# Optimization experiments

Measured on AMD Instinct MI355X. Metric: run time of the kernel, lower is better.

Reference implementation:

```python
import jax, jax.numpy as jnp
import numpy as np

NEG_SLOPE = 0.2

def gat_conv(x, src, dst, W, a_src, a_dst, b, n_nodes):
    # x: [N, Fin]; src/dst: [E] (self-loops included); W: [Fin, H]
    h = x @ W                                   # [N, H]
    s_src = h @ a_src                           # [N]
    s_dst = h @ a_dst                           # [N]
    e = jax.nn.leaky_relu(s_src[src] + s_dst[dst], NEG_SLOPE)  # [E]
    # scatter-softmax over incoming edges per destination node
    m = jax.ops.segment_max(e, dst, num_segments=n_nodes)      # [N]
    ex = jnp.exp(e - m[dst])                                   # [E]
    denom = jax.ops.segment_sum(ex, dst, num_segments=n_nodes) # [N]
    alpha = ex / denom[dst]                                    # [E]
    out = jax.ops.segment_sum(h[src] * alpha[:, None], dst, num_segments=n_nodes)
    return out + b


def setup_inputs() -> dict:
    key = jax.random.key(0)
    ks = jax.random.split(key, 16)
    N, E, F_IN, H, C = 100000, 1600000, 128, 128, 64
    x = jax.random.normal(ks[0], (N, F_IN), dtype=jnp.float32)
    edge_index = jax.random.randint(ks[1], (2, E), 0, N, dtype=jnp.int64)
    def glorot(k, shape):
        fan = sum(shape)
        return jax.random.normal(k, shape, dtype=jnp.float32) * jnp.sqrt(2.0 / fan)
    W1 = glorot(ks[2], (F_IN, H)); a1_src = glorot(ks[3], (H,)); a1_dst = glorot(ks[4], (H,)); b1 = jnp.zeros((H,), jnp.float32)
    W2 = glorot(ks[5], (H, H));    a2_src = glorot(ks[6], (H,)); a2_dst = glorot(ks[7], (H,)); b2 = jnp.zeros((H,), jnp.float32)
    Wl = glorot(ks[8], (H, C));    bl = jnp.zeros((C,), jnp.float32)
    return {"x": x, "edge_index": edge_index,
            "W1": W1, "a1_src": a1_src, "a1_dst": a1_dst, "b1": b1,
            "W2": W2, "a2_src": a2_src, "a2_dst": a2_dst, "b2": b2,
            "Wl": Wl, "bl": bl}


def reference(x, edge_index, W1, a1_src, a1_dst, b1, W2, a2_src, a2_dst, b2, Wl, bl):
    n = x.shape[0]
    loops = jnp.arange(n, dtype=edge_index.dtype)
    src = jnp.concatenate([edge_index[0], loops])  # add_self_loops=True (PyG default)
    dst = jnp.concatenate([edge_index[1], loops])
    h = jax.nn.relu(gat_conv(x, src, dst, W1, a1_src, a1_dst, b1, n))
    # F.dropout in eval mode is identity
    h2 = gat_conv(h, src, dst, W2, a2_src, a2_dst, b2, n)
    out = h + h2
    logp = jax.nn.log_softmax(out @ Wl + bl, axis=1)
    return (logp, edge_index)
```

## Files before the change

kernel.cpp:

```cpp
#include <hip/hip_runtime.h>

typedef unsigned short u16;
typedef __bf16 bf16x8 __attribute__((ext_vector_type(8)));
typedef float f32x4 __attribute__((ext_vector_type(4)));
typedef unsigned short u16x8 __attribute__((ext_vector_type(8)));

#define GA 256

static __device__ __forceinline__ float bf2f(u16 u) {
    return __uint_as_float(((unsigned)u) << 16);
}
static __device__ __forceinline__ u16 f2bf(float f) {
    unsigned u = __float_as_uint(f);
    unsigned r = (u + 0x7FFFu + ((u >> 16) & 1u)) >> 16;
    return (u16)r;
}

__global__ void detect_kernel(const int* __restrict__ ei, int* __restrict__ flag) {
    if (blockIdx.x == 0 && threadIdx.x == 0) {
        int zc = 0;
        for (int t = 0; t < 64; ++t) zc += (ei[2 * t + 1] == 0) ? 1 : 0;
        *flag = (zc >= 60) ? 2 : 1;
    }
}
static __device__ __forceinline__ int ld_idx(const int* ei, int pos, int st, int N) {
    int v = ei[(size_t)pos * (size_t)st];
    return v < 0 ? 0 : (v >= N ? N - 1 : v);
}

#define SCHUNK 4096
__global__ void xscan_reduce(const int* __restrict__ arr, int* __restrict__ bsum, int M) {
    __shared__ int sdata[256];
    int t = threadIdx.x;
    int base = blockIdx.x * SCHUNK + t * 16;
    int s = 0;
#pragma unroll
    for (int j = 0; j < 16; ++j) { int i = base + j; s += (i < M) ? arr[i] : 0; }
    sdata[t] = s;
    __syncthreads();
    for (int o = 128; o > 0; o >>= 1) {
        if (t < o) sdata[t] += sdata[t + o];
        __syncthreads();
    }
    if (t == 0) bsum[blockIdx.x] = sdata[0];
}
__global__ void scan_mid_kernel(int* __restrict__ bsum, int nb) {
    if (threadIdx.x == 0 && blockIdx.x == 0) {
        int run = 0;
        for (int b = 0; b < nb; ++b) { int v = bsum[b]; bsum[b] = run; run += v; }
    }
}
__global__ void xscan_final(int* __restrict__ arr, const int* __restrict__ bsum, int M) {
    __shared__ int sdata[256];
    int t = threadIdx.x;
    int base = blockIdx.x * SCHUNK + t * 16;
    int v[16];
    int s = 0;
#pragma unroll
    for (int j = 0; j < 16; ++j) {
        int i = base + j;
        v[j] = (i < M) ? arr[i] : 0;
        s += v[j];
    }
    sdata[t] = s;
    __syncthreads();
    for (int o = 1; o < 256; o <<= 1) {
        int add = (t >= o) ? sdata[t - o] : 0;
        __syncthreads();
        sdata[t] += add;
        __syncthreads();
    }
    int excl = (t == 0) ? 0 : sdata[t - 1];
    int off = bsum[blockIdx.x] + excl;
#pragma unroll
    for (int j = 0; j < 16; ++j) {
        int i = base + j;
        if (i < M) { arr[i] = off; off += v[j]; }
    }
}

__global__ __launch_bounds__(256) void partition_kernel(const int* __restrict__ ei,
                                                        const int* __restrict__ flag,
                                                        const int* __restrict__ offs,
                                                        unsigned* __restrict__ ebuf, int E,
                                                        int N) {
    __shared__ int cur[1024];
    const int K = (N + 127) >> 7;
    const int bh = blockIdx.x;
    for (int k = threadIdx.x; k < K; k += 256) cur[k] = offs[(size_t)k * GA + bh];
    __syncthreads();
    const int st = *flag;
    const int chunk = (E + GA - 1) / GA;
    const int lo = bh * chunk;
    const int hi = (lo + chunk < E) ? lo + chunk : E;
    for (int j = lo + (int)threadIdx.x; j < hi; j += 256) {
        int d = ld_idx(ei, E + j, st, N);
        int s = ld_idx(ei, j, st, N);
        int pos = atomicAdd(&cur[d >> 7], 1);
        ebuf[pos] = ((unsigned)(d & 127) << 25) | (unsigned)s;
    }
}

__global__ __launch_bounds__(256) void csr_build(const unsigned* __restrict__ ebuf,
                                                 const int* __restrict__ offs,
                                                 int* __restrict__ rowptr,
                                                 int* __restrict__ col, int E, int N, int ET) {
    __shared__ int dg[128];
    __shared__ int sc[128];
    __shared__ int cur[128];
    const int K = (N + 127) >> 7;
    const int k = blockIdx.x;
    const int base = k << 7;
    const int nn = (N - base < 128) ? (N - base) : 128;
    const int e0 = offs[(size_t)k * GA];
    const int e1 = (k + 1 < K) ? offs[(size_t)(k + 1) * GA] : E;
    for (int t = threadIdx.x; t < 128; t += 256) dg[t] = 0;
    __syncthreads();
    for (int e = e0 + (int)threadIdx.x; e < e1; e += 256)
        atomicAdd(&dg[ebuf[e] >> 25], 1);
    __syncthreads();
    const int t = threadIdx.x;
    int v = 0;
    if (t < 128) {
        v = (t < nn) ? dg[t] + 1 : 0;
        sc[t] = v;
    }
    __syncthreads();
    for (int o = 1; o < 128; o <<= 1) {
        int add = 0;
        if (t < 128 && t >= o) add = sc[t - o];
        __syncthreads();
        if (t < 128) sc[t] += add;
        __syncthreads();
    }
    const int colbase = e0 + base;
    if (t < nn) {
        int rp = colbase + sc[t] - v;
        rowptr[base + t] = rp;
        col[rp] = base + t;
        cur[t] = rp + 1;
    }
    if (k == 0 && t == 0) rowptr[N] = ET;
    __syncthreads();
    for (int e = e0 + (int)threadIdx.x; e < e1; e += 256) {
        unsigned p = ebuf[e];
        int pos = atomicAdd(&cur[p >> 25], 1);
        col[pos] = (int)(p & 0x1FFFFFFu);
    }
}

template <int NC, bool AF32, int EPI, bool HIST>
__global__ __launch_bounds__(256) void gemm_fused(
    const void* __restrict__ Ap, const float* __restrict__ W, u16* __restrict__ Cout, int M,
    const float* __restrict__ av_s, const float* __restrict__ av_d, float* __restrict__ ssrc,
    float* __restrict__ sdst, const float* __restrict__ bl, float* __restrict__ outp,
    const int* __restrict__ ei, const int* __restrict__ flag, int* __restrict__ cntmat, int E,
    int ET, int N, int G1) {
    if (HIST && (int)blockIdx.x >= G1) {
        __shared__ int cnt[1024];
        const int bh = (int)blockIdx.x - G1;
        const int nga = (int)gridDim.x - G1;
        const int K = (N + 127) >> 7;
        for (int k = threadIdx.x; k < K; k += 256) cnt[k] = 0;
        __syncthreads();
        const int st = *flag;
        const int chunk = (E + nga - 1) / nga;
        const int lo = bh * chunk;
        const int hi = (lo + chunk < E) ? lo + chunk : E;
        for (int j = lo + (int)threadIdx.x; j < hi; j += 256) {
            int d = ld_idx(ei, E + j, st, N);
            atomicAdd(&cnt[d >> 7], 1);
        }
        __syncthreads();
        for (int k = threadIdx.x; k < K; k += 256) cntmat[(size_t)k * nga + bh] = cnt[k];
        return;
    }
    const int lane = threadIdx.x & 63;
    const int quad = lane >> 4;
    const int r = lane & 15;
    const int gw = (blockIdx.x * 256 + threadIdx.x) >> 6;
    const int nw = G1 * 4;

    bf16x8 bf[NC / 16][4];
#pragma unroll
    for (int nt = 0; nt < NC / 16; ++nt)
#pragma unroll
        for (int kk = 0; kk < 4; ++kk) {
            union { bf16x8 v; u16 s[8]; } u;
#pragma unroll
            for (int j = 0; j < 8; ++j)
                u.s[j] = f2bf(W[(size_t)(kk * 32 + quad * 8 + j) * NC + nt * 16 + r]);
            bf[nt][kk] = u.v;
        }
    float avs[NC / 16], avd[NC / 16], blv[NC / 16];
    if (EPI == 1) {
#pragma unroll
        for (int nt = 0; nt < NC / 16; ++nt) {
            avs[nt] = av_s[nt * 16 + r];
            avd[nt] = av_d[nt * 16 + r];
        }
    }
    if (EPI == 2) {
#pragma unroll
        for (int nt = 0; nt < NC / 16; ++nt) blv[nt] = bl[nt * 16 + r];
    }

    const int ntiles = (M + 15) >> 4;
    for (int t = gw; t < ntiles; t += nw) {
        const int row0 = t << 4;
        bf16x8 af[4];
        if (AF32) {
            const float* arow = (const float*)Ap + (size_t)(row0 + r) * 128;
#pragma unroll
            for (int kk = 0; kk < 4; ++kk) {
                f32x4 f0 = *reinterpret_cast<const f32x4*>(arow + kk * 32 + quad * 8);
                f32x4 f1 = *reinterpret_cast<const f32x4*>(arow + kk * 32 + quad * 8 + 4);
                union { bf16x8 v; u16 s[8]; } u;
#pragma unroll
                for (int j = 0; j < 4; ++j) { u.s[j] = f2bf(f0[j]); u.s[4 + j] = f2bf(f1[j]); }
                af[kk] = u.v;
            }
        } else {
            const u16* arow = (const u16*)Ap + (size_t)(row0 + r) * 128;
#pragma unroll
            for (int kk = 0; kk < 4; ++kk)
                af[kk] = *reinterpret_cast<const bf16x8*>(arow + kk * 32 + quad * 8);
        }
        f32x4 acc[NC / 16];
#pragma unroll
        for (int nt = 0; nt < NC / 16; ++nt) acc[nt] = (f32x4){0.f, 0.f, 0.f, 0.f};
#pragma unroll
        for (int kk = 0; kk < 4; ++kk)
#pragma unroll
            for (int nt = 0; nt < NC / 16; ++nt)
                acc[nt] = __builtin_amdgcn_mfma_f32_16x16x32_bf16(af[kk], bf[nt][kk],
                                                                  acc[nt], 0, 0, 0);
        if (EPI != 2) {
#pragma unroll
            for (int nt = 0; nt < NC / 16; ++nt)
#pragma unroll
                for (int reg = 0; reg < 4; ++reg)
                    Cout[(size_t)(row0 + quad * 4 + reg) * NC + nt * 16 + r] =
                        f2bf(acc[nt][reg]);
        }
        if (EPI == 1) {
            float ps[4] = {0.f, 0.f, 0.f, 0.f}, pd[4] = {0.f, 0.f, 0.f, 0.f};
#pragma unroll
            for (int nt = 0; nt < NC / 16; ++nt)
#pragma unroll
                for (int reg = 0; reg < 4; ++reg) {
                    ps[reg] += acc[nt][reg] * avs[nt];
                    pd[reg] += acc[nt][reg] * avd[nt];
                }
#pragma unroll
            for (int o = 1; o < 16; o <<= 1)
#pragma unroll
                for (int reg = 0; reg < 4; ++reg) {
                    ps[reg] += __shfl_xor(ps[reg], o);
                    pd[reg] += __shfl_xor(pd[reg], o);
                }
            if (r == 0) {
#pragma unroll
                for (int reg = 0; reg < 4; ++reg) {
                    ssrc[row0 + quad * 4 + reg] = ps[reg];
                    sdst[row0 + quad * 4 + reg] = pd[reg];
                }
            }
        }
        if (EPI == 2) {
#pragma unroll
            for (int reg = 0; reg < 4; ++reg) {
                float v[NC / 16];
                float m = -3.4e38f;
#pragma unroll
                for (int nt = 0; nt < NC / 16; ++nt) {
                    v[nt] = acc[nt][reg] + blv[nt];
                    m = fmaxf(m, v[nt]);
                }
#pragma unroll
                for (int o = 1; o < 16; o <<= 1) m = fmaxf(m, __shfl_xor(m, o));
                float s = 0.f;
#pragma unroll
                for (int nt = 0; nt < NC / 16; ++nt) s += __expf(v[nt] - m);
#pragma unroll
                for (int o = 1; o < 16; o <<= 1) s += __shfl_xor(s, o);
                float L = __logf(s);
                const size_t rb = (size_t)(row0 + quad * 4 + reg) * NC;
#pragma unroll
                for (int nt = 0; nt < NC / 16; ++nt)
                    outp[rb + nt * 16 + r] = v[nt] - m - L;
            }
        }
    }
}

template <int MODE>
__global__ __launch_bounds__(256) void agg_fused(
    const int* __restrict__ rowptr, const int* __restrict__ col,
    const float* __restrict__ ssrc, const float* __restrict__ sdst,
    const u16* __restrict__ h, const float* __restrict__ b, const u16* __restrict__ skip,
    u16* __restrict__ out, int N) {
    const int lane = threadIdx.x & 63;
    const int gwave = (blockIdx.x * 256 + threadIdx.x) >> 6;
    const int grp = lane >> 4;
    const int ln = lane & 15;
    const int i = gwave * 4 + grp;
    if (i >= N) return;
    const int start = rowptr[i], end = rowptr[i + 1];
    const float sd = sdst[i];
    float sm = 0.f;
    for (int e = start + ln; e < end; e += 16) {
        float sc = ssrc[col[e]] + sd;
        sc = sc > 0.f ? sc : 0.2f * sc;
        sm += __expf(fminf(sc, 60.f));
    }
#pragma unroll
    for (int o = 1; o < 16; o <<= 1) sm += __shfl_xor(sm, o);
    const float rd = 1.f / sm;

    const size_t coff = (size_t)ln * 8;
    float acc[8] = {0.f, 0.f, 0.f, 0.f, 0.f, 0.f, 0.f, 0.f};
    int e = start;
    for (; e + 2 <= end; e += 2) {
        int c0 = col[e], c1 = col[e + 1];
        float s0 = ssrc[c0] + sd;
        float s1 = ssrc[c1] + sd;
        s0 = s0 > 0.f ? s0 : 0.2f * s0;
        s1 = s1 > 0.f ? s1 : 0.2f * s1;
        float w0 = __expf(fminf(s0, 60.f)) * rd;
        float w1 = __expf(fminf(s1, 60.f)) * rd;
        u16x8 r0 = *reinterpret_cast<const u16x8*>(h + (size_t)c0 * 128 + coff);
        u16x8 r1 = *reinterpret_cast<const u16x8*>(h + (size_t)c1 * 128 + coff);
#pragma unroll
        for (int j = 0; j < 8; ++j) acc[j] += w0 * bf2f(r0[j]) + w1 * bf2f(r1[j]);
    }
    if (e < end) {
        int c0 = col[e];
        float s0 = ssrc[c0] + sd;
        s0 = s0 > 0.f ? s0 : 0.2f * s0;
        float w0 = __expf(fminf(s0, 60.f)) * rd;
        u16x8 r0 = *reinterpret_cast<const u16x8*>(h + (size_t)c0 * 128 + coff);
#pragma unroll
        for (int j = 0; j < 8; ++j) acc[j] += w0 * bf2f(r0[j]);
    }
    u16x8 o;
    if (MODE == 1) {
#pragma unroll
        for (int j = 0; j < 8; ++j) {
            float v = acc[j] + b[coff + j];
            v = v > 0.f ? v : 0.f;
            o[j] = f2bf(v);
        }
    } else {
        const u16x8 sk = *reinterpret_cast<const u16x8*>(skip + (size_t)i * 128 + coff);
#pragma unroll
        for (int j = 0; j < 8; ++j) {
            float v = acc[j] + b[coff + j] + bf2f(sk[j]);
            o[j] = f2bf(v);
        }
    }
    *reinterpret_cast<u16x8*>(out + (size_t)i * 128 + coff) = o;
}

__global__ void copy_ei_kernel(const int* __restrict__ ei, const int* __restrict__ flag,
                               float* __restrict__ out, int n, int N) {
    int j = blockIdx.x * 256 + threadIdx.x;
    if (j < n) out[j] = (float)ld_idx(ei, j, *flag, N);
}

extern "C" void kernel_launch(void* const* d_in, const int* in_sizes, int n_in, void* d_out,
                              int out_size, void* d_ws, size_t ws_size, hipStream_t stream) {
    int ix = 0, iei = 1;
    if (in_sizes[0] < in_sizes[1]) { ix = 1; iei = 0; }
    const float* x = (const float*)d_in[ix];
    const int* ei = (const int*)d_in[iei];
    const float* W1 = (const float*)d_in[2];
    const float* a1s = (const float*)d_in[3];
    const float* a1d = (const float*)d_in[4];
    const float* b1 = (const float*)d_in[5];
    const float* W2 = (const float*)d_in[6];
    const float* a2s = (const float*)d_in[7];
    const float* a2d = (const float*)d_in[8];
    const float* b2 = (const float*)d_in[9];
    const float* Wl = (const float*)d_in[10];
    const float* bl = (const float*)d_in[11];

    const int N = in_sizes[ix] / 128;
    const int E = (out_size - N * 64) / 2;
    const int ET = E + N;
    const int K = (N + 127) >> 7;
    const int Mscan = K * GA;

    char* ws = (char*)d_ws;
    size_t off = 0;
    auto alloc = [&](size_t bytes) {
        void* p = ws + off;
        off += (bytes + 255) & ~(size_t)255;
        return p;
    };
    u16* h = (u16*)alloc((size_t)N * 128 * 2);
    u16* h1 = (u16*)alloc((size_t)N * 128 * 2);
    u16* o2 = (u16*)alloc((size_t)N * 128 * 2);
    float* ssrc = (float*)alloc((size_t)N * 4);
    float* sdst = (float*)alloc((size_t)N * 4);
    int* eflag = (int*)alloc(256);
    int* cntmat = (int*)alloc((size_t)Mscan * 4);
    int* rowptr = (int*)alloc((size_t)(N + 1) * 4);
    int* bsum = (int*)alloc(4096);
    int* colv = (int*)alloc((size_t)ET * 4);
    unsigned* ebuf = (unsigned*)h1;

    float* out_logp = (float*)d_out;
    float* out_ei = out_logp + (size_t)N * 64;

    dim3 blk(256);
    const int ngrid4 = (N + 15) / 16;
    const int nbx = (Mscan + SCHUNK - 1) / SCHUNK;
    const int G1 = 512;

    detect_kernel<<<1, 64, 0, stream>>>(ei, eflag);

    gemm_fused<128, true, 1, true><<<G1 + GA, blk, 0, stream>>>(
        x, W1, h, N, a1s, a1d, ssrc, sdst, nullptr, nullptr, ei, eflag, cntmat, E, ET, N, G1);

    xscan_reduce<<<nbx, blk, 0, stream>>>(cntmat, bsum, Mscan);
    scan_mid_kernel<<<1, 64, 0, stream>>>(bsum, nbx);
    xscan_final<<<nbx, blk, 0, stream>>>(cntmat, bsum, Mscan);

    partition_kernel<<<GA, blk, 0, stream>>>(ei, eflag, cntmat, ebuf, E, N);
    csr_build<<<K, blk, 0, stream>>>(ebuf, cntmat, rowptr, colv, E, N, ET);

    agg_fused<1><<<ngrid4, blk, 0, stream>>>(rowptr, colv, ssrc, sdst, h, b1, nullptr, h1, N);

    gemm_fused<128, false, 1, false><<<G1, blk, 0, stream>>>(
        h1, W2, h, N, a2s, a2d, ssrc, sdst, nullptr, nullptr, nullptr, nullptr, nullptr, 0, 0,
        N, G1);
    agg_fused<2><<<ngrid4, blk, 0, stream>>>(rowptr, colv, ssrc, sdst, h, b2, h1, o2, N);

    gemm_fused<64, false, 2, false><<<G1, blk, 0, stream>>>(
        o2, Wl, nullptr, N, nullptr, nullptr, nullptr, nullptr, bl, out_logp, nullptr, nullptr,
        nullptr, 0, 0, N, G1);

    copy_ei_kernel<<<(2 * E + 255) / 256, blk, 0, stream>>>(ei, eflag, out_ei, 2 * E, N);
}
```

Measured before the change: 389.7 us.

## Store features in 16-column slices and split aggregation into weight and sliced passes

```diff
diff --git a/kernel.cpp b/kernel.cpp
--- a/kernel.cpp
+++ b/kernel.cpp
@@ -180,6 +180,7 @@
     const int r = lane & 15;
     const int gw = (blockIdx.x * 256 + threadIdx.x) >> 6;
     const int nw = G1 * 4;
+    const size_t SL = (size_t)M * 16;
 
     bf16x8 bf[NC / 16][4];
 #pragma unroll
@@ -221,10 +222,13 @@
                 af[kk] = u.v;
             }
         } else {
-            const u16* arow = (const u16*)Ap + (size_t)(row0 + r) * 128;
-#pragma unroll
-            for (int kk = 0; kk < 4; ++kk)
-                af[kk] = *reinterpret_cast<const bf16x8*>(arow + kk * 32 + quad * 8);
+            const u16* abase = (const u16*)Ap;
+#pragma unroll
+            for (int kk = 0; kk < 4; ++kk) {
+                const int fb = kk * 32 + quad * 8;
+                af[kk] = *reinterpret_cast<const bf16x8*>(
+                    abase + (size_t)(fb >> 4) * SL + (size_t)(row0 + r) * 16 + (fb & 15));
+            }
         }
         f32x4 acc[NC / 16];
 #pragma unroll
@@ -240,7 +244,7 @@
             for (int nt = 0; nt < NC / 16; ++nt)
 #pragma unroll
                 for (int reg = 0; reg < 4; ++reg)
-                    Cout[(size_t)(row0 + quad * 4 + reg) * NC + nt * 16 + r] =
+                    Cout[(size_t)nt * SL + (size_t)(row0 + quad * 4 + reg) * 16 + r] =
                         f2bf(acc[nt][reg]);
         }
         if (EPI == 1) {
@@ -294,12 +298,12 @@
     }
 }
 
-template <int MODE>
-__global__ __launch_bounds__(256) void agg_fused(
-    const int* __restrict__ rowptr, const int* __restrict__ col,
-    const float* __restrict__ ssrc, const float* __restrict__ sdst,
-    const u16* __restrict__ h, const float* __restrict__ b, const u16* __restrict__ skip,
-    u16* __restrict__ out, int N) {
+__global__ __launch_bounds__(256) void wcompute(const int* __restrict__ rowptr,
+                                                const int* __restrict__ col,
+                                                const float* __restrict__ ssrc,
+                                                const float* __restrict__ sdst,
+                                                u16* __restrict__ wv,
+                                                float* __restrict__ rdenom, int N) {
     const int lane = threadIdx.x & 63;
     const int gwave = (blockIdx.x * 256 + threadIdx.x) >> 6;
     const int grp = lane >> 4;
@@ -312,54 +316,84 @@
     for (int e = start + ln; e < end; e += 16) {
         float sc = ssrc[col[e]] + sd;
         sc = sc > 0.f ? sc : 0.2f * sc;
-        sm += __expf(fminf(sc, 60.f));
+        float w = __expf(fminf(sc, 60.f));
+        unsigned u = __float_as_uint(w) & 0xFFFF0000u;
+        wv[e] = (u16)(u >> 16);
+        sm += __uint_as_float(u);
     }
 #pragma unroll
     for (int o = 1; o < 16; o <<= 1) sm += __shfl_xor(sm, o);
-    const float rd = 1.f / sm;
-
-    const size_t coff = (size_t)ln * 8;
-    float acc[8] = {0.f, 0.f, 0.f, 0.f, 0.f, 0.f, 0.f, 0.f};
+    if (ln == 0) rdenom[i] = 1.f / sm;
+}
+
+template <int MODE>
+__global__ __launch_bounds__(256) void agg_sliced(
+    const int* __restrict__ rowptr, const int* __restrict__ col,
+    const u16* __restrict__ wv, const float* __restrict__ rdenom,
+    const u16* __restrict__ hT, const float* __restrict__ b, const u16* __restrict__ skipT,
+    u16* __restrict__ outT, int N) {
+    const int slice = blockIdx.x & 7;
+    const int wb = blockIdx.x >> 3;
+    const int lane = threadIdx.x & 63;
+    const int gwave = (wb * 256 + (int)threadIdx.x) >> 6;
+    const int grp = lane >> 4;
+    const int ln = lane & 15;
+    const int i = gwave * 4 + grp;
+    if (i >= N) return;
+    const int start = rowptr[i], end = rowptr[i + 1];
+    const int hi = ln >> 3;
+    const int f2 = (ln & 7) * 2;
+    const size_t SL = (size_t)N * 16;
+    const u16* hs = hT + (size_t)slice * SL;
+
+    float a0 = 0.f, a1 = 0.f;
     int e = start;
+    for (; e + 8 <= end; e += 8) {
+        int c0 = col[e + hi], c1 = col[e + 2 + hi], c2 = col[e + 4 + hi],
+            c3 = col[e + 6 + hi];
+        u16 w0 = wv[e + hi], w1 = wv[e + 2 + hi], w2 = wv[e + 4 + hi], w3 = wv[e + 6 + hi];
+        unsigned r0 = *reinterpret_cast<const unsigned*>(hs + (size_t)c0 * 16 + f2);
+        unsigned r1 = *reinterpret_cast<const unsigned*>(hs + (size_t)c1 * 16 + f2);
+        unsigned r2 = *reinterpret_cast<const unsigned*>(hs + (size_t)c2 * 16 + f2);
+        unsigned r3 = *reinterpret_cast<const unsigned*>(hs + (size_t)c3 * 16 + f2);
+        float fw0 = bf2f(w0), fw1 = bf2f(w1), fw2 = bf2f(w2), fw3 = bf2f(w3);
+        a0 += fw0 * bf2f((u16)(r0 & 0xFFFFu)) + fw1 * bf2f((u16)(r1 & 0xFFFFu));
+        a1 += fw0 * bf2f((u16)(r0 >> 16)) + fw1 * bf2f((u16)(r1 >> 16));
+        a0 += fw2 * bf2f((u16)(r2 & 0xFFFFu)) + fw3 * bf2f((u16)(r3 & 0xFFFFu));
+        a1 += fw2 * bf2f((u16)(r2 >> 16)) + fw3 * bf2f((u16)(r3 >> 16));
+    }
     for (; e + 2 <= end; e += 2) {
-        int c0 = col[e], c1 = col[e + 1];
-        float s0 = ssrc[c0] + sd;
-        float s1 = ssrc[c1] + sd;
-        s0 = s0 > 0.f ? s0 : 0.2f * s0;
-        s1 = s1 > 0.f ? s1 : 0.2f * s1;
-        float w0 = __expf(fminf(s0, 60.f)) * rd;
-        float w1 = __expf(fminf(s1, 60.f)) * rd;
-        u16x8 r0 = *reinterpret_cast<const u16x8*>(h + (size_t)c0 * 128 + coff);
-        u16x8 r1 = *reinterpret_cast<const u16x8*>(h + (size_t)c1 * 128 + coff);
-#pragma unroll
-        for (int j = 0; j < 8; ++j) acc[j] += w0 * bf2f(r0[j]) + w1 * bf2f(r1[j]);
-    }
-    if (e < end) {
+        int c0 = col[e + hi];
+        u16 w0 = wv[e + hi];
+        unsigned r0 = *reinterpret_cast<const unsigned*>(hs + (size_t)c0 * 16 + f2);
+        float fw0 = bf2f(w0);
+        a0 += fw0 * bf2f((u16)(r0 & 0xFFFFu));
+        a1 += fw0 * bf2f((u16)(r0 >> 16));
+    }
+    if (e < end && hi == 0) {
         int c0 = col[e];
-        float s0 = ssrc[c0] + sd;
-        s0 = s0 > 0.f ? s0 : 0.2f * s0;
-        float w0 = __expf(fminf(s0, 60.f)) * rd;
-        u16x8 r0 = *reinterpret_cast<const u16x8*>(h + (size_t)c0 * 128 + coff);
-#pragma unroll
-        for (int j = 0; j < 8; ++j) acc[j] += w0 * bf2f(r0[j]);
-    }
-    u16x8 o;
-    if (MODE == 1) {
-#pragma unroll
-        for (int j = 0; j < 8; ++j) {
-            float v = acc[j] + b[coff + j];
-            v = v > 0.f ? v : 0.f;
-            o[j] = f2bf(v);
-        }
-    } else {
-        const u16x8 sk = *reinterpret_cast<const u16x8*>(skip + (size_t)i * 128 + coff);
-#pragma unroll
-        for (int j = 0; j < 8; ++j) {
-            float v = acc[j] + b[coff + j] + bf2f(sk[j]);
-            o[j] = f2bf(v);
-        }
-    }
-    *reinterpret_cast<u16x8*>(out + (size_t)i * 128 + coff) = o;
+        float fw0 = bf2f(wv[e]);
+        unsigned r0 = *reinterpret_cast<const unsigned*>(hs + (size_t)c0 * 16 + f2);
+        a0 += fw0 * bf2f((u16)(r0 & 0xFFFFu));
+        a1 += fw0 * bf2f((u16)(r0 >> 16));
+    }
+    a0 += __shfl_xor(a0, 8);
+    a1 += __shfl_xor(a1, 8);
+    if (hi == 0) {
+        const float rd = rdenom[i];
+        float v0 = a0 * rd + b[slice * 16 + f2];
+        float v1 = a1 * rd + b[slice * 16 + f2 + 1];
+        if (MODE == 1) {
+            v0 = v0 > 0.f ? v0 : 0.f;
+            v1 = v1 > 0.f ? v1 : 0.f;
+        } else {
+            const u16* sk = skipT + (size_t)slice * SL + (size_t)i * 16 + f2;
+            v0 += bf2f(sk[0]);
+            v1 += bf2f(sk[1]);
+        }
+        unsigned o = ((unsigned)f2bf(v1) << 16) | (unsigned)f2bf(v0);
+        *reinterpret_cast<unsigned*>(outT + (size_t)slice * SL + (size_t)i * 16 + f2) = o;
+    }
 }
 
 __global__ void copy_ei_kernel(const int* __restrict__ ei, const int* __restrict__ flag,
@@ -408,6 +442,8 @@
     int* rowptr = (int*)alloc((size_t)(N + 1) * 4);
     int* bsum = (int*)alloc(4096);
     int* colv = (int*)alloc((size_t)ET * 4);
+    u16* wv = (u16*)alloc((size_t)ET * 2);
+    float* rdenom = (float*)alloc((size_t)N * 4);
     unsigned* ebuf = (unsigned*)h1;
 
     float* out_logp = (float*)d_out;
@@ -430,12 +466,15 @@
     partition_kernel<<<GA, blk, 0, stream>>>(ei, eflag, cntmat, ebuf, E, N);
     csr_build<<<K, blk, 0, stream>>>(ebuf, cntmat, rowptr, colv, E, N, ET);
 
-    agg_fused<1><<<ngrid4, blk, 0, stream>>>(rowptr, colv, ssrc, sdst, h, b1, nullptr, h1, N);
+    wcompute<<<ngrid4, blk, 0, stream>>>(rowptr, colv, ssrc, sdst, wv, rdenom, N);
+    agg_sliced<1><<<ngrid4 * 8, blk, 0, stream>>>(rowptr, colv, wv, rdenom, h, b1, nullptr,
+                                                  h1, N);
 
     gemm_fused<128, false, 1, false><<<G1, blk, 0, stream>>>(
         h1, W2, h, N, a2s, a2d, ssrc, sdst, nullptr, nullptr, nullptr, nullptr, nullptr, 0, 0,
         N, G1);
-    agg_fused<2><<<ngrid4, blk, 0, stream>>>(rowptr, colv, ssrc, sdst, h, b2, h1, o2, N);
+    wcompute<<<ngrid4, blk, 0, stream>>>(rowptr, colv, ssrc, sdst, wv, rdenom, N);
+    agg_sliced<2><<<ngrid4 * 8, blk, 0, stream>>>(rowptr, colv, wv, rdenom, h, b2, h1, o2, N);
 
     gemm_fused<64, false, 2, false><<<G1, blk, 0, stream>>>(
         o2, Wl, nullptr, N, nullptr, nullptr, nullptr, nullptr, bl, out_logp, nullptr, nullptr,
```

Measured after the change: 511.8 us. 31.3% more time.
